# Optimization experiments

Measured on AMD Instinct MI355X. Metric: run time of the kernel, lower is better.

## Reference

```python
import jax, jax.numpy as jnp
import numpy as np

E = 1024   # embed_dim
H = 16     # num_heads
D = E // H # head_dim = 64
HD2 = D // 2
B = 2
S = 2048


def setup_inputs() -> dict:
    key = jax.random.key(0)
    ks = jax.random.split(key, 12)
    def lin(k, fan_in, fan_out):
        # xavier-uniform-ish init, stored in [in, out] (jax) convention
        lim = float(np.sqrt(6.0 / (fan_in + fan_out)))
        return jax.random.uniform(k, (fan_in, fan_out), jnp.float32, -lim, lim)
    return {
        "query": jax.random.normal(ks[0], (B, S, E), jnp.float32),
        "xi_scale": jax.random.uniform(ks[1], (B,), jnp.float32),
        "Wq": lin(ks[2], E, E), "bq": jnp.zeros((E,), jnp.float32),
        "Wk": lin(ks[3], E, E), "bk": jnp.zeros((E,), jnp.float32),
        "Wv": lin(ks[4], E, E), "bv": jnp.zeros((E,), jnp.float32),
        "Wo": lin(ks[5], E, E), "bo": jnp.zeros((E,), jnp.float32),
        "enc_w1": lin(ks[6], 1, HD2), "enc_b1": jnp.zeros((HD2,), jnp.float32),
        "ln_g": jnp.ones((HD2,), jnp.float32), "ln_b": jnp.zeros((HD2,), jnp.float32),
        "enc_w2": lin(ks[7], HD2, D), "enc_b2": jnp.zeros((D,), jnp.float32),
        "scale_gating": jnp.ones((H,), jnp.float32),
    }


def reference(query, xi_scale, Wq, bq, Wk, bk, Wv, bv, Wo, bo,
              enc_w1, enc_b1, ln_g, ln_b, enc_w2, enc_b2, scale_gating):
    b, s, e = query.shape
    h, d = H, e // H
    # --- scale adaptation: xi -> Linear -> LayerNorm -> GELU -> Linear ---
    x = xi_scale[:, None] @ enc_w1 + enc_b1                  # [B, D/2]
    mu = x.mean(-1, keepdims=True)
    var = ((x - mu) ** 2).mean(-1, keepdims=True)
    x = (x - mu) / jnp.sqrt(var + 1e-5) * ln_g + ln_b
    x = jax.nn.gelu(x, approximate=False)
    xe = x @ enc_w2 + enc_b2                                 # [B, D]
    adapt = 1.0 + jax.nn.sigmoid(scale_gating)[None, :, None] * xe[:, None, :]  # [B, H, D]
    # --- projections (self-attention: key = value = query) ---
    q = (query @ Wq + bq).reshape(b, s, h, d).transpose(0, 2, 1, 3) * adapt[:, :, None, :]
    k = (query @ Wk + bk).reshape(b, s, h, d).transpose(0, 2, 1, 3) * adapt[:, :, None, :]
    v = (query @ Wv + bv).reshape(b, s, h, d).transpose(0, 2, 1, 3)
    # --- explicit QK^T / sqrt(d) -> softmax -> V ---
    inv_scale = 1.0 / float(np.sqrt(d))
    scores = jnp.einsum('bhqd,bhkd->bhqk', q, k) * inv_scale  # [B, H, S, S]
    attn = jax.nn.softmax(scores, axis=-1)
    out = jnp.einsum('bhqk,bhkd->bhqd', attn, v)              # [B, H, S, D]
    out = out.transpose(0, 2, 1, 3).reshape(b, s, e)
    return out @ Wo + bo
```

## Files before the change

kernel.cpp:

```cpp
#include <hip/hip_runtime.h>

typedef __bf16 bf16;
typedef __attribute__((ext_vector_type(8))) __bf16 bf16x8;
typedef __attribute__((ext_vector_type(4))) float f32x4;
typedef __attribute__((ext_vector_type(16))) float f32x16;
typedef unsigned int u32;

#define MFMA16(a, b, c) __builtin_amdgcn_mfma_f32_16x16x32_bf16((a), (b), (c), 0, 0, 0)
#define MFMA32(a, b, c) __builtin_amdgcn_mfma_f32_32x32x16_bf16((a), (b), (c), 0, 0, 0)

#define BB 2
#define SS 2048
#define EE 1024
#define HH 16
#define DD 64
#define MM (BB * SS)

__device__ inline f32x4 zero4() {
    f32x4 z; z.x = 0.f; z.y = 0.f; z.z = 0.f; z.w = 0.f; return z;
}

__device__ __forceinline__ void gload16(const bf16* g, bf16* l) {
    __builtin_amdgcn_global_load_lds(
        (const __attribute__((address_space(1))) u32*)(const void*)g,
        (__attribute__((address_space(3))) u32*)(void*)l,
        16, 0, 0);
}

__device__ __forceinline__ u32 pkbf(float a, float b) {
    union { __bf16 h; unsigned short s; } ua, ub;
    ua.h = (__bf16)a; ub.h = (__bf16)b;
    return (u32)ua.s | ((u32)ub.s << 16);
}

__global__ __launch_bounds__(256) void prep_kernel(
    const float* __restrict__ query, bf16* __restrict__ qc,
    const float* __restrict__ s0, const float* __restrict__ s1,
    const float* __restrict__ s2, const float* __restrict__ s3,
    bf16* __restrict__ d0, bf16* __restrict__ d1,
    bf16* __restrict__ d2, bf16* __restrict__ d3,
    const float* __restrict__ xi, const float* __restrict__ w1,
    const float* __restrict__ b1, const float* __restrict__ lng,
    const float* __restrict__ lnb, const float* __restrict__ w2,
    const float* __restrict__ b2, const float* __restrict__ gate,
    float* __restrict__ adapt) {
    __shared__ bf16 tile[64 * 72];
    const int bid = blockIdx.x;
    const int t = threadIdx.x;

    if (bid < 2048) {
        const int i = (bid * 256 + t) * 8;
        float4 a = *(const float4*)(query + i);
        float4 b = *(const float4*)(query + i + 4);
        bf16 tmp[8];
        tmp[0] = (bf16)a.x; tmp[1] = (bf16)a.y; tmp[2] = (bf16)a.z; tmp[3] = (bf16)a.w;
        tmp[4] = (bf16)b.x; tmp[5] = (bf16)b.y; tmp[6] = (bf16)b.z; tmp[7] = (bf16)b.w;
        *(uint4*)(qc + i) = *(uint4*)tmp;
    } else if (bid < 3072) {
        const int m = (bid - 2048) >> 8;
        const int idx0 = (bid - 2048) & 255;
        const float* W = (m == 0) ? s0 : (m == 1) ? s1 : (m == 2) ? s2 : s3;
        bf16* Wt = (m == 0) ? d0 : (m == 1) ? d1 : (m == 2) ? d2 : d3;
        const int k0 = (idx0 >> 4) * 64, n0 = (idx0 & 15) * 64;
#pragma unroll
        for (int i = 0; i < 2; ++i) {
            int idx = i * 256 + t;
            int r = idx >> 3, c = (idx & 7) * 8;
            float4 a = *(const float4*)(W + (k0 + r) * EE + n0 + c);
            float4 b = *(const float4*)(W + (k0 + r) * EE + n0 + c + 4);
            bf16 tmp[8];
            tmp[0] = (bf16)a.x; tmp[1] = (bf16)a.y; tmp[2] = (bf16)a.z; tmp[3] = (bf16)a.w;
            tmp[4] = (bf16)b.x; tmp[5] = (bf16)b.y; tmp[6] = (bf16)b.z; tmp[7] = (bf16)b.w;
            *(uint4*)(tile + r * 72 + c) = *(uint4*)tmp;
        }
        __syncthreads();
#pragma unroll
        for (int i = 0; i < 2; ++i) {
            int idx = i * 256 + t;
            int n = idx >> 3, kc = (idx & 7) * 8;
            bf16 tmp[8];
#pragma unroll
            for (int j = 0; j < 8; ++j) tmp[j] = tile[(kc + j) * 72 + n];
            *(uint4*)(Wt + (n0 + n) * EE + k0 + kc) = *(uint4*)tmp;
        }
    } else {
        const int b = bid - 3072;
        float* xs = (float*)tile;
        if (t < 64) {
            const float xiv = xi[b];
            float xv = 0.f;
            if (t < 32) xv = xiv * w1[t] + b1[t];
            float sm = xv;
            for (int off = 1; off < 32; off <<= 1) sm += __shfl_xor(sm, off);
            const float mu = sm * (1.f / 32.f);
            float dv = (t < 32) ? (xv - mu) : 0.f;
            float s2 = dv * dv;
            for (int off = 1; off < 32; off <<= 1) s2 += __shfl_xor(s2, off);
            const float var = s2 * (1.f / 32.f);
            if (t < 32) {
                float xn = (xv - mu) * rsqrtf(var + 1e-5f) * lng[t] + lnb[t];
                float ge = 0.5f * xn * (1.f + erff(xn * 0.70710678118654752f));
                xs[t] = ge;
            }
        }
        __syncthreads();
        if (t < 64) {
            float acc = b2[t];
            for (int j = 0; j < 32; ++j) acc += xs[j] * w2[j * DD + t];
            for (int h = 0; h < HH; ++h) {
                float sg = 1.f / (1.f + __expf(-gate[h]));
                adapt[(b * HH + h) * DD + t] = 1.f + sg * acc;
            }
        }
    }
}

__global__ __launch_bounds__(256, 3) void gemm_qkv(
    const bf16* __restrict__ Aq, const bf16* __restrict__ Bqk,
    const bf16* __restrict__ Av,
    const float* __restrict__ bias, const float* __restrict__ bias2,
    const float* __restrict__ bias3, const float* __restrict__ adapt,
    bf16* __restrict__ outqk, bf16* __restrict__ outvt) {
    __shared__ bf16 As[2 * 128 * 32];
    __shared__ bf16 Bs[2 * 128 * 32];

    const int t = threadIdx.x;
    const int w = t >> 6, lane = t & 63;
    const int mrow = lane & 15, quad = lane >> 4;
    const int wm = (w & 1) * 64, wn = (w >> 1) * 64;

    int md, bx, by;
    const bf16 *Ap, *Bp;
    int bid = blockIdx.x;
    if (bid < 512) { md = 5; bx = bid & 31; by = bid >> 5; Ap = Aq; Bp = Bqk; }
    else { md = 4; bid -= 512; bx = bid & 7; by = bid >> 3; Ap = Av; Bp = Aq; }
    const int m0 = bx * 128, n0 = by * 128;

    f32x4 acc[4][4];
#pragma unroll
    for (int i = 0; i < 4; ++i)
#pragma unroll
        for (int j = 0; j < 4; ++j) acc[i][j] = zero4();

    const int dr = lane >> 2;
    const int dcg = ((lane & 3) ^ (dr & 3)) * 8;
    const bf16* Ag = Ap + (size_t)(m0 + w * 16 + dr) * EE + dcg;
    const bf16* Bg = Bp + (size_t)(n0 + w * 16 + dr) * EE + dcg;
    bf16* Al = As + (w * 16) * 32;
    bf16* Bl = Bs + (w * 16) * 32;

    gload16(Ag, Al);
    gload16(Ag + 64 * EE, Al + 64 * 32);
    gload16(Bg, Bl);
    gload16(Bg + 64 * EE, Bl + 64 * 32);

    for (int kt = 0; kt < 32; ++kt) {
        __syncthreads();
        if (kt < 31) {
            const int kn = (kt + 1) * 32;
            const int nb = (kt + 1) & 1;
            gload16(Ag + kn, Al + nb * 4096);
            gload16(Ag + 64 * EE + kn, Al + nb * 4096 + 64 * 32);
            gload16(Bg + kn, Bl + nb * 4096);
            gload16(Bg + 64 * EE + kn, Bl + nb * 4096 + 64 * 32);
        }
        const bf16* Ab = As + (kt & 1) * 4096;
        const bf16* Bb = Bs + (kt & 1) * 4096;
        const int sw = (quad ^ (mrow & 3)) * 8;
        bf16x8 af[4], bfr[4];
#pragma unroll
        for (int i = 0; i < 4; ++i)
            af[i] = *(const bf16x8*)(Ab + (wm + i * 16 + mrow) * 32 + sw);
#pragma unroll
        for (int j = 0; j < 4; ++j)
            bfr[j] = *(const bf16x8*)(Bb + (wn + j * 16 + mrow) * 32 + sw);
#pragma unroll
        for (int i = 0; i < 4; ++i)
#pragma unroll
            for (int j = 0; j < 4; ++j)
                acc[i][j] = MFMA16(af[i], bfr[j], acc[i][j]);
    }

#pragma unroll
    for (int i = 0; i < 4; ++i) {
#pragma unroll
        for (int j = 0; j < 4; ++j) {
            const int col = n0 + wn + j * 16 + mrow;
#pragma unroll
            for (int r = 0; r < 4; ++r) {
                const int row = m0 + wm + i * 16 + quad * 4 + r;
                float v = acc[i][j][r];
                if (md == 4) {
                    v += bias3[row];
                    const int h = row >> 6, d = row & 63;
                    const int b = col >> 11, s = col & (SS - 1);
                    outvt[(((b * HH + h) * DD + d) * SS) + s] = (bf16)v;
                } else {
                    const int m2 = col >> 10;
                    const int cl = col & 1023;
                    const int h = cl >> 6, d = cl & 63;
                    const int b = row >> 11, s = row & (SS - 1);
                    v += (m2 ? bias2[cl] : bias[cl]);
                    v *= adapt[(b * HH + h) * DD + d];
                    if (!m2) v *= 0.18033688011113811f;
                    outqk[(size_t)m2 * MM * EE + ((b * HH + h) * SS + s) * DD + d] = (bf16)v;
                }
            }
        }
    }
}

__global__ __launch_bounds__(256, 3) void gemm_o(
    const bf16* __restrict__ A, const bf16* __restrict__ Bt,
    const float* __restrict__ bias, float* __restrict__ outf) {
    __shared__ bf16 As[2 * 128 * 64];
    __shared__ bf16 Bs[2 * 64 * 64];

    const int t = threadIdx.x;
    const int w = t >> 6, lane = t & 63;
    const int mrow = lane & 15, quad = lane >> 4;
    const int m0 = blockIdx.x * 128, n0 = blockIdx.y * 64;

    f32x4 acc[2][4];
#pragma unroll
    for (int i = 0; i < 2; ++i)
#pragma unroll
        for (int j = 0; j < 4; ++j) acc[i][j] = zero4();

    const int grow = lane >> 3;
    const int gsw = ((lane & 7) ^ grow) * 8;
    const bf16* Ag = A + (size_t)(m0 + w * 32 + grow) * EE + gsw;
    const bf16* Bg = Bt + (size_t)(n0 + w * 16 + grow) * EE + gsw;
    bf16* Al = As + (w * 32) * 64;
    bf16* Bl = Bs + (w * 16) * 64;

#pragma unroll
    for (int i = 0; i < 4; ++i) gload16(Ag + i * 8 * EE, Al + i * 8 * 64);
#pragma unroll
    for (int i = 0; i < 2; ++i) gload16(Bg + i * 8 * EE, Bl + i * 8 * 64);

    for (int kt = 0; kt < 16; ++kt) {
        __syncthreads();
        if (kt < 15) {
            const int kn = (kt + 1) * 64;
            const int nb = (kt + 1) & 1;
#pragma unroll
            for (int i = 0; i < 4; ++i)
                gload16(Ag + i * 8 * EE + kn, Al + nb * 8192 + i * 8 * 64);
#pragma unroll
            for (int i = 0; i < 2; ++i)
                gload16(Bg + i * 8 * EE + kn, Bl + nb * 4096 + i * 8 * 64);
        }
        const bf16* Ab = As + (kt & 1) * 8192;
        const bf16* Bb = Bs + (kt & 1) * 4096;
#pragma unroll
        for (int ks = 0; ks < 2; ++ks) {
            const int cg = ks * 4 + quad;
            const int sw = (cg ^ (mrow & 7)) * 8;
            bf16x8 af[2], bfr[4];
#pragma unroll
            for (int mi = 0; mi < 2; ++mi)
                af[mi] = *(const bf16x8*)(Ab + (w * 32 + mi * 16 + mrow) * 64 + sw);
#pragma unroll
            for (int nj = 0; nj < 4; ++nj)
                bfr[nj] = *(const bf16x8*)(Bb + (nj * 16 + mrow) * 64 + sw);
#pragma unroll
            for (int mi = 0; mi < 2; ++mi)
#pragma unroll
                for (int nj = 0; nj < 4; ++nj)
                    acc[mi][nj] = MFMA16(af[mi], bfr[nj], acc[mi][nj]);
        }
    }

#pragma unroll
    for (int mi = 0; mi < 2; ++mi) {
#pragma unroll
        for (int nj = 0; nj < 4; ++nj) {
            const int col = n0 + nj * 16 + mrow;
#pragma unroll
            for (int r = 0; r < 4; ++r) {
                const int row = m0 + w * 32 + mi * 16 + quad * 4 + r;
                outf[row * EE + col] = acc[mi][nj][r] + bias[col];
            }
        }
    }
}

__global__ __launch_bounds__(256, 2) void attn_kernel(
    const bf16* __restrict__ q, const bf16* __restrict__ k,
    const bf16* __restrict__ vt, bf16* __restrict__ o0) {
    __shared__ bf16 lds[16896];
    bf16* Ks = lds;
    bf16* Vs = lds + 8192;

    const int t = threadIdx.x;
    const int w = t >> 6, lane = t & 63;
    const int q32 = lane & 31, h = lane >> 5;
    const int bh = blockIdx.x & 31;
    const int qb = blockIdx.x >> 5;
    const int qr0 = qb * 256 + w * 64;

    bf16x8 qf[2][4];
#pragma unroll
    for (int qi = 0; qi < 2; ++qi)
#pragma unroll
        for (int c = 0; c < 4; ++c)
            qf[qi][c] = *(const bf16x8*)(q + (size_t)(bh * SS + qr0 + qi * 32 + q32) * DD +
                                         c * 16 + h * 8);

    f32x16 oacc[2][2];
#pragma unroll
    for (int qi = 0; qi < 2; ++qi)
#pragma unroll
        for (int mf = 0; mf < 2; ++mf)
#pragma unroll
            for (int i = 0; i < 16; ++i) oacc[qi][mf][i] = 0.f;
    float lsum[2] = {0.f, 0.f};

    const int dr = lane >> 3;
    const int dcg = ((lane & 7) ^ dr) * 8;
    const bf16* kg = k + (size_t)bh * SS * DD;
    const bf16* vg = vt + (size_t)bh * DD * SS;
    const bf16* kgl = kg + (size_t)dr * DD + dcg;
    const bf16* vgl = vg + (size_t)(w * 16 + dr) * SS + dcg;

#pragma unroll
    for (int i = 0; i < 2; ++i) {
        const int rb = w * 16 + i * 8;
        gload16(kgl + (size_t)rb * DD, Ks + rb * 64);
        gload16(vgl + (size_t)(i * 8) * SS, Vs + rb * 64);
    }

    for (int kt = 0; kt < SS / 64; ++kt) {
        __syncthreads();
        if (kt < SS / 64 - 1) {
            const int nb = (kt + 1) & 1;
#pragma unroll
            for (int i = 0; i < 2; ++i) {
                const int rb = w * 16 + i * 8;
                gload16(kgl + (size_t)((kt + 1) * 64 + rb) * DD, Ks + nb * 4096 + rb * 64);
                gload16(vgl + (size_t)(i * 8) * SS + (kt + 1) * 64, Vs + nb * 4096 + rb * 64);
            }
        }
        const bf16* Kb = Ks + (kt & 1) * 4096;
        const bf16* Vb = Vs + (kt & 1) * 4096;

        f32x16 st[2][2];
#pragma unroll
        for (int qi = 0; qi < 2; ++qi)
#pragma unroll
            for (int mf = 0; mf < 2; ++mf)
#pragma unroll
                for (int i = 0; i < 16; ++i) st[qi][mf][i] = 0.f;
#pragma unroll
        for (int c = 0; c < 4; ++c) {
            const int sw = ((2 * c + h) ^ (q32 & 7)) * 8;
#pragma unroll
            for (int mf = 0; mf < 2; ++mf) {
                bf16x8 kf = *(const bf16x8*)(Kb + (mf * 32 + q32) * 64 + sw);
#pragma unroll
                for (int qi = 0; qi < 2; ++qi)
                    st[qi][mf] = MFMA32(kf, qf[qi][c], st[qi][mf]);
            }
        }

        u32 P32[2][2][8];
#pragma unroll
        for (int qi = 0; qi < 2; ++qi)
#pragma unroll
            for (int mf = 0; mf < 2; ++mf)
#pragma unroll
                for (int rp = 0; rp < 8; ++rp) {
                    float pa = __builtin_amdgcn_exp2f(st[qi][mf][2 * rp]);
                    float pb = __builtin_amdgcn_exp2f(st[qi][mf][2 * rp + 1]);
                    lsum[qi] += pa + pb;
                    P32[qi][mf][rp] = pkbf(pa, pb);
                }

#pragma unroll
        for (int c = 0; c < 4; ++c) {
            const int mfs = c >> 1;
            const int ro = (c & 1) * 4;
            union { u32 u[4]; bf16x8 v; } pb[2];
#pragma unroll
            for (int qi = 0; qi < 2; ++qi) {
                u32 vA0 = P32[qi][mfs][ro + 0], vA1 = P32[qi][mfs][ro + 1];
                u32 vB0 = P32[qi][mfs][ro + 2], vB1 = P32[qi][mfs][ro + 3];
                u32 prep0 = h ? vA0 : vB0;
                u32 prep1 = h ? vA1 : vB1;
                u32 sh0 = __shfl_xor(prep0, 32);
                u32 sh1 = __shfl_xor(prep1, 32);
                pb[qi].u[0] = h ? sh0 : vA0;
                pb[qi].u[1] = h ? sh1 : vA1;
                pb[qi].u[2] = h ? vB0 : sh0;
                pb[qi].u[3] = h ? vB1 : sh1;
            }
            const int sw = ((2 * c + h) ^ (q32 & 7)) * 8;
#pragma unroll
            for (int mf = 0; mf < 2; ++mf) {
                bf16x8 vf = *(const bf16x8*)(Vb + (mf * 32 + q32) * 64 + sw);
#pragma unroll
                for (int qi = 0; qi < 2; ++qi)
                    oacc[qi][mf] = MFMA32(vf, pb[qi].v, oacc[qi][mf]);
            }
        }
    }

    lsum[0] += __shfl_xor(lsum[0], 32);
    lsum[1] += __shfl_xor(lsum[1], 32);
    const float inv[2] = {1.f / lsum[0], 1.f / lsum[1]};

    __syncthreads();
    bf16* ob = lds + w * 4224;
#pragma unroll
    for (int qi = 0; qi < 2; ++qi)
#pragma unroll
        for (int mf = 0; mf < 2; ++mf)
#pragma unroll
            for (int rp = 0; rp < 8; ++rp) {
                const int d = 32 * mf + 2 * (rp & 1) + 8 * (rp >> 1) + 4 * h;
                *(u32*)(ob + (qi * 32 + q32) * 66 + d) =
                    pkbf(oacc[qi][mf][2 * rp] * inv[qi],
                         oacc[qi][mf][2 * rp + 1] * inv[qi]);
            }
    __syncthreads();

    const int b = bh >> 4, head = bh & 15;
    const int half = lane & 1;
#pragma unroll
    for (int p = 0; p < 2; ++p) {
        const int r = p * 32 + (lane >> 1);
#pragma unroll
        for (int i = 0; i < 4; ++i) {
            bf16x8 val = *(const bf16x8*)(ob + r * 66 + half * 32 + i * 8);
            *(bf16x8*)(o0 + (size_t)(b * SS + qr0 + r) * EE + head * DD +
                       half * 32 + i * 8) = val;
        }
    }
}

extern "C" void kernel_launch(void* const* d_in, const int* in_sizes, int n_in,
                              void* d_out, int out_size, void* d_ws, size_t ws_size,
                              hipStream_t stream) {
    const float* query = (const float*)d_in[0];
    const float* xi    = (const float*)d_in[1];
    const float* Wq = (const float*)d_in[2];  const float* bq = (const float*)d_in[3];
    const float* Wk = (const float*)d_in[4];  const float* bk = (const float*)d_in[5];
    const float* Wv = (const float*)d_in[6];  const float* bv = (const float*)d_in[7];
    const float* Wo = (const float*)d_in[8];  const float* bo = (const float*)d_in[9];
    const float* ew1 = (const float*)d_in[10]; const float* eb1 = (const float*)d_in[11];
    const float* lng = (const float*)d_in[12]; const float* lnb = (const float*)d_in[13];
    const float* ew2 = (const float*)d_in[14]; const float* eb2 = (const float*)d_in[15];
    const float* gate = (const float*)d_in[16];
    float* out = (float*)d_out;

    char* ws = (char*)d_ws;
    const size_t SZ = (size_t)MM * EE * sizeof(bf16);
    const size_t WSZ = (size_t)EE * EE * sizeof(bf16);

    bf16* queryc = (bf16*)(ws);
    bf16* p0     = (bf16*)(ws);
    bf16* qws    = (bf16*)(ws + SZ);
    bf16* kws    = (bf16*)(ws + 2 * SZ);
    bf16* vtws   = (bf16*)(ws + 3 * SZ);
    bf16* wqT    = (bf16*)(ws + 4 * SZ);
    bf16* wkT    = (bf16*)(ws + 4 * SZ + WSZ);
    bf16* wvT    = (bf16*)(ws + 4 * SZ + 2 * WSZ);
    bf16* woT    = (bf16*)(ws + 4 * SZ + 3 * WSZ);
    float* adaptws = (float*)(ws + 4 * SZ + 4 * WSZ);

    prep_kernel<<<3074, 256, 0, stream>>>(query, queryc, Wq, Wk, Wv, Wo,
                                          wqT, wkT, wvT, woT,
                                          xi, ew1, eb1, lng, lnb, ew2, eb2, gate,
                                          adaptws);

    gemm_qkv<<<768, 256, 0, stream>>>(queryc, wqT, wvT, bq, bk, bv, adaptws,
                                      qws, vtws);

    attn_kernel<<<256, 256, 0, stream>>>(qws, kws, vtws, p0);

    gemm_o<<<dim3(MM / 128, EE / 64), 256, 0, stream>>>(p0, woT, bo, out);
}
```

Measured before the change: 218.3 us.

## Halve per-wave query rows in attention to double block count

Each wave in the attention kernel now handles 32 query rows instead of 64, so a block covers 128 queries and the grid grows from 256 to 512 blocks. This gives more blocks than the 256 CUs and lowers register pressure per wave. In exchange, every K/V tile loaded into LDS is reused by half as many query rows, which doubles total K/V global and LDS traffic. The output staging buffer in LDS shrinks to match.

```diff
diff --git a/kernel.cpp b/kernel.cpp
--- a/kernel.cpp
+++ b/kernel.cpp
@@ -289,7 +289,7 @@
 __global__ __launch_bounds__(256, 2) void attn_kernel(
     const bf16* __restrict__ q, const bf16* __restrict__ k,
     const bf16* __restrict__ vt, bf16* __restrict__ o0) {
-    __shared__ bf16 lds[16896];
+    __shared__ bf16 lds[16384];
     bf16* Ks = lds;
     bf16* Vs = lds + 8192;
 
@@ -298,24 +298,19 @@
     const int q32 = lane & 31, h = lane >> 5;
     const int bh = blockIdx.x & 31;
     const int qb = blockIdx.x >> 5;
-    const int qr0 = qb * 256 + w * 64;
-
-    bf16x8 qf[2][4];
-#pragma unroll
-    for (int qi = 0; qi < 2; ++qi)
-#pragma unroll
-        for (int c = 0; c < 4; ++c)
-            qf[qi][c] = *(const bf16x8*)(q + (size_t)(bh * SS + qr0 + qi * 32 + q32) * DD +
-                                         c * 16 + h * 8);
-
-    f32x16 oacc[2][2];
-#pragma unroll
-    for (int qi = 0; qi < 2; ++qi)
-#pragma unroll
-        for (int mf = 0; mf < 2; ++mf)
-#pragma unroll
-            for (int i = 0; i < 16; ++i) oacc[qi][mf][i] = 0.f;
-    float lsum[2] = {0.f, 0.f};
+    const int qr0 = qb * 128 + w * 32;
+
+    bf16x8 qf[4];
+#pragma unroll
+    for (int c = 0; c < 4; ++c)
+        qf[c] = *(const bf16x8*)(q + (size_t)(bh * SS + qr0 + q32) * DD + c * 16 + h * 8);
+
+    f32x16 oacc[2];
+#pragma unroll
+    for (int mf = 0; mf < 2; ++mf)
+#pragma unroll
+        for (int i = 0; i < 16; ++i) oacc[mf][i] = 0.f;
+    float lsum = 0.f;
 
     const int dr = lane >> 3;
     const int dcg = ((lane & 7) ^ dr) * 8;
@@ -345,97 +340,81 @@
         const bf16* Kb = Ks + (kt & 1) * 4096;
         const bf16* Vb = Vs + (kt & 1) * 4096;
 
-        f32x16 st[2][2];
-#pragma unroll
-        for (int qi = 0; qi < 2; ++qi)
-#pragma unroll
-            for (int mf = 0; mf < 2; ++mf)
-#pragma unroll
-                for (int i = 0; i < 16; ++i) st[qi][mf][i] = 0.f;
+        f32x16 st[2];
+#pragma unroll
+        for (int mf = 0; mf < 2; ++mf)
+#pragma unroll
+            for (int i = 0; i < 16; ++i) st[mf][i] = 0.f;
 #pragma unroll
         for (int c = 0; c < 4; ++c) {
             const int sw = ((2 * c + h) ^ (q32 & 7)) * 8;
 #pragma unroll
             for (int mf = 0; mf < 2; ++mf) {
                 bf16x8 kf = *(const bf16x8*)(Kb + (mf * 32 + q32) * 64 + sw);
-#pragma unroll
-                for (int qi = 0; qi < 2; ++qi)
-                    st[qi][mf] = MFMA32(kf, qf[qi][c], st[qi][mf]);
-            }
-        }
-
-        u32 P32[2][2][8];
-#pragma unroll
-        for (int qi = 0; qi < 2; ++qi)
-#pragma unroll
-            for (int mf = 0; mf < 2; ++mf)
-#pragma unroll
-                for (int rp = 0; rp < 8; ++rp) {
-                    float pa = __builtin_amdgcn_exp2f(st[qi][mf][2 * rp]);
-                    float pb = __builtin_amdgcn_exp2f(st[qi][mf][2 * rp + 1]);
-                    lsum[qi] += pa + pb;
-                    P32[qi][mf][rp] = pkbf(pa, pb);
-                }
+                st[mf] = MFMA32(kf, qf[c], st[mf]);
+            }
+        }
+
+        u32 P32[2][8];
+#pragma unroll
+        for (int mf = 0; mf < 2; ++mf)
+#pragma unroll
+            for (int rp = 0; rp < 8; ++rp) {
+                float pa = __builtin_amdgcn_exp2f(st[mf][2 * rp]);
+                float pb = __builtin_amdgcn_exp2f(st[mf][2 * rp + 1]);
+                lsum += pa + pb;
+                P32[mf][rp] = pkbf(pa, pb);
+            }
 
 #pragma unroll
         for (int c = 0; c < 4; ++c) {
             const int mfs = c >> 1;
             const int ro = (c & 1) * 4;
-            union { u32 u[4]; bf16x8 v; } pb[2];
-#pragma unroll
-            for (int qi = 0; qi < 2; ++qi) {
-                u32 vA0 = P32[qi][mfs][ro + 0], vA1 = P32[qi][mfs][ro + 1];
-                u32 vB0 = P32[qi][mfs][ro + 2], vB1 = P32[qi][mfs][ro + 3];
+            union { u32 u[4]; bf16x8 v; } pb;
+            {
+                u32 vA0 = P32[mfs][ro + 0], vA1 = P32[mfs][ro + 1];
+                u32 vB0 = P32[mfs][ro + 2], vB1 = P32[mfs][ro + 3];
                 u32 prep0 = h ? vA0 : vB0;
                 u32 prep1 = h ? vA1 : vB1;
                 u32 sh0 = __shfl_xor(prep0, 32);
                 u32 sh1 = __shfl_xor(prep1, 32);
-                pb[qi].u[0] = h ? sh0 : vA0;
-                pb[qi].u[1] = h ? sh1 : vA1;
-                pb[qi].u[2] = h ? vB0 : sh0;
-                pb[qi].u[3] = h ? vB1 : sh1;
+                pb.u[0] = h ? sh0 : vA0;
+                pb.u[1] = h ? sh1 : vA1;
+                pb.u[2] = h ? vB0 : sh0;
+                pb.u[3] = h ? vB1 : sh1;
             }
             const int sw = ((2 * c + h) ^ (q32 & 7)) * 8;
 #pragma unroll
             for (int mf = 0; mf < 2; ++mf) {
                 bf16x8 vf = *(const bf16x8*)(Vb + (mf * 32 + q32) * 64 + sw);
-#pragma unroll
-                for (int qi = 0; qi < 2; ++qi)
-                    oacc[qi][mf] = MFMA32(vf, pb[qi].v, oacc[qi][mf]);
-            }
-        }
-    }
-
-    lsum[0] += __shfl_xor(lsum[0], 32);
-    lsum[1] += __shfl_xor(lsum[1], 32);
-    const float inv[2] = {1.f / lsum[0], 1.f / lsum[1]};
+                oacc[mf] = MFMA32(vf, pb.v, oacc[mf]);
+            }
+        }
+    }
+
+    lsum += __shfl_xor(lsum, 32);
+    const float inv = 1.f / lsum;
 
     __syncthreads();
-    bf16* ob = lds + w * 4224;
-#pragma unroll
-    for (int qi = 0; qi < 2; ++qi)
-#pragma unroll
-        for (int mf = 0; mf < 2; ++mf)
-#pragma unroll
-            for (int rp = 0; rp < 8; ++rp) {
-                const int d = 32 * mf + 2 * (rp & 1) + 8 * (rp >> 1) + 4 * h;
-                *(u32*)(ob + (qi * 32 + q32) * 66 + d) =
-                    pkbf(oacc[qi][mf][2 * rp] * inv[qi],
-                         oacc[qi][mf][2 * rp + 1] * inv[qi]);
-            }
+    bf16* ob = lds + w * 2112;
+#pragma unroll
+    for (int mf = 0; mf < 2; ++mf)
+#pragma unroll
+        for (int rp = 0; rp < 8; ++rp) {
+            const int d = 32 * mf + 2 * (rp & 1) + 8 * (rp >> 1) + 4 * h;
+            *(u32*)(ob + q32 * 66 + d) =
+                pkbf(oacc[mf][2 * rp] * inv, oacc[mf][2 * rp + 1] * inv);
+        }
     __syncthreads();
 
     const int b = bh >> 4, head = bh & 15;
     const int half = lane & 1;
-#pragma unroll
-    for (int p = 0; p < 2; ++p) {
-        const int r = p * 32 + (lane >> 1);
-#pragma unroll
-        for (int i = 0; i < 4; ++i) {
-            bf16x8 val = *(const bf16x8*)(ob + r * 66 + half * 32 + i * 8);
-            *(bf16x8*)(o0 + (size_t)(b * SS + qr0 + r) * EE + head * DD +
-                       half * 32 + i * 8) = val;
-        }
+    const int r = lane >> 1;
+#pragma unroll
+    for (int i = 0; i < 4; ++i) {
+        bf16x8 val = *(const bf16x8*)(ob + r * 66 + half * 32 + i * 8);
+        *(bf16x8*)(o0 + (size_t)(b * SS + qr0 + r) * EE + head * DD +
+                   half * 32 + i * 8) = val;
     }
 }
 
@@ -477,7 +456,7 @@
     gemm_qkv<<<768, 256, 0, stream>>>(queryc, wqT, wvT, bq, bk, bv, adaptws,
                                       qws, vtws);
 
-    attn_kernel<<<256, 256, 0, stream>>>(qws, kws, vtws, p0);
+    attn_kernel<<<512, 256, 0, stream>>>(qws, kws, vtws, p0);
 
     gemm_o<<<dim3(MM / 128, EE / 64), 256, 0, stream>>>(p0, woT, bo, out);
 }
```

After: 217.1 us. Within noise of the previous version (-0.6%).
